# Optimization experiments

Measured on AMD Instinct MI355X. Metric: run time of the kernel, lower is better.

Reference implementation:

```python
import jax, jax.numpy as jnp
import numpy as np

ORDER = 3  # polynomial filter order


def _sketch_conv(x, A, W, b, coeffs):
    # z = A @ (x W + b); out = sum_d coeffs[d-1] * z**d  (Horner-free power accumulation)
    z = A @ (x @ W + b)            # [N, out_c]
    p = z
    acc = coeffs[0] * z
    for d in range(1, ORDER):      # small fixed loop over polynomial order
        p = p * z
        acc = acc + coeffs[d] * p
    return acc


def setup_inputs() -> dict:
    key = jax.random.key(0)
    ks = jax.random.split(key, 12)
    N, C_IN, C_H, C_OUT = 8192, 128, 64, 40
    nf_mats = jax.random.normal(ks[0], (N, C_IN), dtype=jnp.float32)
    # scale by 1/sqrt(N) so polynomial powers stay O(1)
    conv_mats = jax.random.normal(ks[1], (N, N), dtype=jnp.float32) / np.float32(np.sqrt(N))
    def lin(k, fi, fo):
        kw, kb = jax.random.split(k)
        W = jax.random.normal(kw, (fi, fo), dtype=jnp.float32) / np.float32(np.sqrt(fi))
        b = jax.random.normal(kb, (fo,), dtype=jnp.float32) * np.float32(0.01)
        return W, b
    W1, b1 = lin(ks[2], C_IN, C_H)
    W2, b2 = lin(ks[3], C_H, C_H)
    W3, b3 = lin(ks[4], C_H, C_OUT)
    base = jnp.array([1.0, 0.0, 0.0], dtype=jnp.float32)
    c1 = base + jax.random.normal(ks[5], (ORDER,), dtype=jnp.float32) * 0.05
    c2 = base + jax.random.normal(ks[6], (ORDER,), dtype=jnp.float32) * 0.05
    c3 = base + jax.random.normal(ks[7], (ORDER,), dtype=jnp.float32) * 0.05
    return {"nf_mats": nf_mats, "conv_mats": conv_mats,
            "W1": W1, "b1": b1, "c1": c1,
            "W2": W2, "b2": b2, "c2": c2,
            "W3": W3, "b3": b3, "c3": c3}


def reference(nf_mats, conv_mats, W1, b1, c1, W2, b2, c2, W3, b3, c3):
    # SketchGCN eval-mode forward: batchnorm=False, dropout inactive.
    x = _sketch_conv(nf_mats, conv_mats, W1, b1, c1)      # first layer
    x = x + _sketch_conv(x, conv_mats, W2, b2, c2)        # residual middle layer
    return _sketch_conv(x, conv_mats, W3, b3, c3)         # output layer
```

## Files before the change

kernel.cpp:

```cpp
#include <hip/hip_runtime.h>
#include <stdint.h>

typedef __bf16 bf16x8 __attribute__((ext_vector_type(8)));
typedef float f32x4 __attribute__((ext_vector_type(4)));

using gvoid = const __attribute__((address_space(1))) void;
using lvoid = __attribute__((address_space(3))) void;

__device__ __forceinline__ unsigned short f2bf(float f) {
    union { float f; unsigned u; } x; x.f = f;
    unsigned u = x.u;
    u += 0x7FFFu + ((u >> 16) & 1u);
    return (unsigned short)(u >> 16);
}
__device__ __forceinline__ unsigned pack2(float lo, float hi) {
    return ((unsigned)f2bf(hi) << 16) | (unsigned)f2bf(lo);
}

template <int CIN>
__global__ __launch_bounds__(256) void small_gemm(const float* __restrict__ X,
                                                  const float* __restrict__ W,
                                                  const float* __restrict__ b,
                                                  int cout,
                                                  unsigned short* __restrict__ Yt) {
    __shared__ float Xs[64 * (CIN + 1)];
    __shared__ float Ws[CIN * 64];
    __shared__ float bs[64];
    const int t = threadIdx.x;
    const int i0 = blockIdx.x * 64;

    for (int e = t; e < 64 * CIN; e += 256) {
        int r = e / CIN, c = e % CIN;
        Xs[r * (CIN + 1) + c] = X[(size_t)(i0 + r) * CIN + c];
    }
    for (int e = t; e < CIN * 64; e += 256) {
        int k = e >> 6, j = e & 63;
        Ws[e] = (j < cout) ? W[k * cout + j] : 0.0f;
    }
    if (t < 64) bs[t] = (t < cout) ? b[t] : 0.0f;
    __syncthreads();

    const int i = t & 63;
    const int jg = t >> 6;
    float acc[16];
#pragma unroll
    for (int jj = 0; jj < 16; ++jj) acc[jj] = 0.0f;

    for (int k = 0; k < CIN; ++k) {
        float xv = Xs[i * (CIN + 1) + k];
        const float4* wr = (const float4*)&Ws[k * 64 + jg * 16];
#pragma unroll
        for (int q = 0; q < 4; ++q) {
            float4 w = wr[q];
            acc[q * 4 + 0] += xv * w.x;
            acc[q * 4 + 1] += xv * w.y;
            acc[q * 4 + 2] += xv * w.z;
            acc[q * 4 + 3] += xv * w.w;
        }
    }
#pragma unroll
    for (int jj = 0; jj < 16; ++jj) {
        int j = jg * 16 + jj;
        Yt[(size_t)j * 8192 + i0 + i] = f2bf(acc[jj] + bs[j]);
    }
}

template <int CONV>
__global__ __launch_bounds__(256) void big_gemm(const float* __restrict__ Afp,
                                                unsigned short* __restrict__ Ab,
                                                const unsigned short* __restrict__ Yt,
                                                float* __restrict__ P) {
    __shared__ unsigned short As[2][128 * 64];
    __shared__ unsigned short Bs[2][64 * 64];
    const int t = threadIdx.x;
    const int lane = t & 63, wid = t >> 6;
    const int lane15 = lane & 15, lane4 = lane >> 4;
    const int wm = wid >> 1, wn = wid & 1;
    const int row0 = blockIdx.x * 128;
    const int kbase = blockIdx.y * 1024;

    f32x4 acc[4][2];
    const f32x4 z4 = {0.f, 0.f, 0.f, 0.f};
#pragma unroll
    for (int m = 0; m < 4; ++m)
#pragma unroll
        for (int n = 0; n < 2; ++n) acc[m][n] = z4;

    float4 ra[4][2];

    auto loadA_regs = [&](int kt) {
#pragma unroll
        for (int ii = 0; ii < 4; ++ii) {
            int p = ii * 256 + t;
            int r = p >> 3, cl = p & 7;
            const float* gp = Afp + (size_t)(row0 + r) * 8192 + kt + cl * 8;
            ra[ii][0] = *(const float4*)gp;
            ra[ii][1] = *(const float4*)(gp + 4);
        }
    };
    auto writeA = [&](int nb, int kt) {
#pragma unroll
        for (int ii = 0; ii < 4; ++ii) {
            int p = ii * 256 + t;
            int r = p >> 3, cl = p & 7;
            uint4 ch;
            ch.x = pack2(ra[ii][0].x, ra[ii][0].y);
            ch.y = pack2(ra[ii][0].z, ra[ii][0].w);
            ch.z = pack2(ra[ii][1].x, ra[ii][1].y);
            ch.w = pack2(ra[ii][1].z, ra[ii][1].w);
            *(uint4*)&As[nb][((r << 3) | (cl ^ (r & 7))) << 3] = ch;
            *(uint4*)&Ab[(size_t)(row0 + r) * 8192 + kt + cl * 8] = ch;
        }
    };
    auto stageA = [&](int nb, int kt) {
#pragma unroll
        for (int ii = 0; ii < 4; ++ii) {
            int p = ii * 256 + wid * 64 + lane;
            int r = p >> 3;
            int c = (p & 7) ^ (r & 7);
            const unsigned short* gp = Ab + (size_t)(row0 + r) * 8192 + (kt + c * 8);
            unsigned short* lp = &As[nb][(ii * 256 + wid * 64) * 8];
            __builtin_amdgcn_global_load_lds((gvoid*)gp, (lvoid*)lp, 16, 0, 0);
        }
    };
    auto stageB = [&](int nb, int kt) {
#pragma unroll
        for (int ii = 0; ii < 2; ++ii) {
            int q = ii * 256 + wid * 64 + lane;
            int n = q >> 3;
            int c = (q & 7) ^ (n & 7);
            const unsigned short* gp = Yt + (size_t)n * 8192 + (kt + c * 8);
            unsigned short* lp = &Bs[nb][(ii * 256 + wid * 64) * 8];
            __builtin_amdgcn_global_load_lds((gvoid*)gp, (lvoid*)lp, 16, 0, 0);
        }
    };

    if (CONV) {
        loadA_regs(kbase);
        stageB(0, kbase);
        writeA(0, kbase);
    } else {
        stageA(0, kbase);
        stageB(0, kbase);
    }
    __syncthreads();

    int buf = 0;
    const int NIT = 16;
    for (int tt = 0; tt < NIT; ++tt) {
        const bool pre = (tt + 1 < NIT);
        const int kt1 = kbase + (tt + 1) * 64;
        if (pre) {
            if (CONV) {
                loadA_regs(kt1);
                stageB(buf ^ 1, kt1);
            } else {
                stageA(buf ^ 1, kt1);
                stageB(buf ^ 1, kt1);
            }
        }
#pragma unroll
        for (int ks = 0; ks < 2; ++ks) {
            bf16x8 af[4], bfr[2];
#pragma unroll
            for (int m = 0; m < 4; ++m) {
                int r = wm * 64 + m * 16 + lane15;
                int c = ks * 4 + lane4;
                af[m] = *(const bf16x8*)&As[buf][((r << 3) | (c ^ (r & 7))) << 3];
            }
#pragma unroll
            for (int n = 0; n < 2; ++n) {
                int rn = wn * 32 + n * 16 + lane15;
                int c = ks * 4 + lane4;
                bfr[n] = *(const bf16x8*)&Bs[buf][((rn << 3) | (c ^ (rn & 7))) << 3];
            }
#pragma unroll
            for (int m = 0; m < 4; ++m)
#pragma unroll
                for (int n = 0; n < 2; ++n)
                    acc[m][n] = __builtin_amdgcn_mfma_f32_16x16x32_bf16(
                        af[m], bfr[n], acc[m][n], 0, 0, 0);
        }
        if (CONV && pre) writeA(buf ^ 1, kt1);
        __syncthreads();
        buf ^= 1;
    }

    float* Po = P + (size_t)blockIdx.y * (8192 * 64);
#pragma unroll
    for (int m = 0; m < 4; ++m) {
        int r = row0 + wm * 64 + m * 16 + lane4 * 4;
#pragma unroll
        for (int n = 0; n < 2; ++n) {
            int cc = wn * 32 + n * 16 + lane15;
#pragma unroll
            for (int q = 0; q < 4; ++q)
                Po[(size_t)(r + q) * 64 + cc] = acc[m][n][q];
        }
    }
}

template <int MODE>
__global__ __launch_bounds__(256) void fused_reduce(const float* __restrict__ P,
                                                    const float* __restrict__ cf,
                                                    const float* __restrict__ Wn,
                                                    const float* __restrict__ bn,
                                                    int cout,
                                                    float* __restrict__ X1,
                                                    unsigned short* __restrict__ Yt) {
    __shared__ float Xs[64 * 65];
    __shared__ float Ws[64 * 64];
    __shared__ float bs[64];
    const int t = threadIdx.x;
    const int i0 = blockIdx.x * 64;
    const size_t NT = 8192 * 64;

    for (int e = t; e < 64 * 64; e += 256) {
        int k = e >> 6, j = e & 63;
        Ws[e] = (j < cout) ? Wn[k * cout + j] : 0.0f;
    }
    if (t < 64) bs[t] = (t < cout) ? bn[t] : 0.0f;
    const float c0 = cf[0], c1 = cf[1], c2 = cf[2];

    for (int s = 0; s < 16; ++s) {
        int e = s * 256 + t;
        int i = e >> 6, j = e & 63;
        size_t base = (size_t)(i0 + i) * 64 + j;
        float z = 0.f;
#pragma unroll
        for (int ks = 0; ks < 8; ++ks) z += P[ks * NT + base];
        float v = z * (c0 + z * (c1 + z * c2));
        if (MODE == 0) X1[base] = v;
        else           v += X1[base];
        Xs[i * 65 + j] = v;
    }
    __syncthreads();

    const int i = t & 63;
    const int jg = t >> 6;
    float acc[16];
#pragma unroll
    for (int jj = 0; jj < 16; ++jj) acc[jj] = 0.0f;
    for (int k = 0; k < 64; ++k) {
        float xv = Xs[i * 65 + k];
        const float4* wr = (const float4*)&Ws[k * 64 + jg * 16];
#pragma unroll
        for (int q = 0; q < 4; ++q) {
            float4 w = wr[q];
            acc[q * 4 + 0] += xv * w.x;
            acc[q * 4 + 1] += xv * w.y;
            acc[q * 4 + 2] += xv * w.z;
            acc[q * 4 + 3] += xv * w.w;
        }
    }
#pragma unroll
    for (int jj = 0; jj < 16; ++jj) {
        int j = jg * 16 + jj;
        Yt[(size_t)j * 8192 + i0 + i] = f2bf(acc[jj] + bs[j]);
    }
}

__global__ void reduce_out(const float* __restrict__ P, const float* __restrict__ cf,
                           float* __restrict__ out) {
    int t = blockIdx.x * 256 + threadIdx.x;
    const size_t NT = 8192 * 64;
    float z = 0.f;
#pragma unroll
    for (int ks = 0; ks < 8; ++ks) z += P[ks * NT + t];
    float c0 = cf[0], c1 = cf[1], c2 = cf[2];
    float v = z * (c0 + z * (c1 + z * c2));
    int i = t >> 6, j = t & 63;
    if (j < 40) out[(size_t)i * 40 + j] = v;
}

extern "C" void kernel_launch(void* const* d_in, const int* in_sizes, int n_in,
                              void* d_out, int out_size, void* d_ws, size_t ws_size,
                              hipStream_t stream) {
    const float* nf   = (const float*)d_in[0];
    const float* Amat = (const float*)d_in[1];
    const float* W1   = (const float*)d_in[2];
    const float* b1   = (const float*)d_in[3];
    const float* c1   = (const float*)d_in[4];
    const float* W2   = (const float*)d_in[5];
    const float* b2   = (const float*)d_in[6];
    const float* c2   = (const float*)d_in[7];
    const float* W3   = (const float*)d_in[8];
    const float* b3   = (const float*)d_in[9];
    const float* c3   = (const float*)d_in[10];
    float* out = (float*)d_out;

    char* ws = (char*)d_ws;
    unsigned short* Abf = (unsigned short*)(ws);
    unsigned short* Yt  = (unsigned short*)(ws + 134217728);
    float* X1           = (float*)(ws + 135266304);
    float* Pp           = (float*)(ws + 137363456);

    small_gemm<128><<<128, 256, 0, stream>>>(nf, W1, b1, 64, Yt);
    big_gemm<1><<<dim3(64, 8), 256, 0, stream>>>(Amat, Abf, Yt, Pp);
    fused_reduce<0><<<128, 256, 0, stream>>>(Pp, c1, W2, b2, 64, X1, Yt);

    big_gemm<0><<<dim3(64, 8), 256, 0, stream>>>(nullptr, Abf, Yt, Pp);
    fused_reduce<1><<<128, 256, 0, stream>>>(Pp, c2, W3, b3, 40, X1, Yt);

    big_gemm<0><<<dim3(64, 8), 256, 0, stream>>>(nullptr, Abf, Yt, Pp);
    reduce_out<<<2048, 256, 0, stream>>>(Pp, c3, out);
}
```

Before: 212.9 us.

## Halve GEMM row tiles for more blocks and vectorize reduction kernels

The row tile of big_gemm drops from 128 to 64, which doubles the grid to 1024 blocks, and launch bounds are added to raise occupancy across the 256 CUs. small_gemm and fused_reduce also use 32-row tiles to double their block counts. The split-K partial-sum reductions in fused_reduce and reduce_out now use float4 loads and stores. Smaller GEMM tiles reload each B tile twice as often, since B reuse per A-load halves, which adds L2 traffic for the bf16 adjacency matrix stream.

```diff
diff --git a/kernel.cpp b/kernel.cpp
--- a/kernel.cpp
+++ b/kernel.cpp
@@ -23,13 +23,13 @@
                                                   const float* __restrict__ b,
                                                   int cout,
                                                   unsigned short* __restrict__ Yt) {
-    __shared__ float Xs[64 * (CIN + 1)];
+    __shared__ float Xs[32 * (CIN + 1)];
     __shared__ float Ws[CIN * 64];
     __shared__ float bs[64];
     const int t = threadIdx.x;
-    const int i0 = blockIdx.x * 64;
-
-    for (int e = t; e < 64 * CIN; e += 256) {
+    const int i0 = blockIdx.x * 32;
+
+    for (int e = t; e < 32 * CIN; e += 256) {
         int r = e / CIN, c = e % CIN;
         Xs[r * (CIN + 1) + c] = X[(size_t)(i0 + r) * CIN + c];
     }
@@ -40,57 +40,55 @@
     if (t < 64) bs[t] = (t < cout) ? b[t] : 0.0f;
     __syncthreads();
 
-    const int i = t & 63;
-    const int jg = t >> 6;
-    float acc[16];
-#pragma unroll
-    for (int jj = 0; jj < 16; ++jj) acc[jj] = 0.0f;
+    const int i = t & 31;
+    const int jg = t >> 5;
+    float acc[8];
+#pragma unroll
+    for (int jj = 0; jj < 8; ++jj) acc[jj] = 0.0f;
 
     for (int k = 0; k < CIN; ++k) {
         float xv = Xs[i * (CIN + 1) + k];
-        const float4* wr = (const float4*)&Ws[k * 64 + jg * 16];
-#pragma unroll
-        for (int q = 0; q < 4; ++q) {
-            float4 w = wr[q];
-            acc[q * 4 + 0] += xv * w.x;
-            acc[q * 4 + 1] += xv * w.y;
-            acc[q * 4 + 2] += xv * w.z;
-            acc[q * 4 + 3] += xv * w.w;
-        }
-    }
-#pragma unroll
-    for (int jj = 0; jj < 16; ++jj) {
-        int j = jg * 16 + jj;
+        const float4* wr = (const float4*)&Ws[k * 64 + jg * 8];
+        float4 w0 = wr[0], w1 = wr[1];
+        acc[0] += xv * w0.x; acc[1] += xv * w0.y;
+        acc[2] += xv * w0.z; acc[3] += xv * w0.w;
+        acc[4] += xv * w1.x; acc[5] += xv * w1.y;
+        acc[6] += xv * w1.z; acc[7] += xv * w1.w;
+    }
+#pragma unroll
+    for (int jj = 0; jj < 8; ++jj) {
+        int j = jg * 8 + jj;
         Yt[(size_t)j * 8192 + i0 + i] = f2bf(acc[jj] + bs[j]);
     }
 }
 
 template <int CONV>
-__global__ __launch_bounds__(256) void big_gemm(const float* __restrict__ Afp,
-                                                unsigned short* __restrict__ Ab,
-                                                const unsigned short* __restrict__ Yt,
-                                                float* __restrict__ P) {
-    __shared__ unsigned short As[2][128 * 64];
+__global__ __launch_bounds__(256, CONV ? 3 : 4)
+void big_gemm(const float* __restrict__ Afp,
+              unsigned short* __restrict__ Ab,
+              const unsigned short* __restrict__ Yt,
+              float* __restrict__ P) {
+    __shared__ unsigned short As[2][64 * 64];
     __shared__ unsigned short Bs[2][64 * 64];
     const int t = threadIdx.x;
     const int lane = t & 63, wid = t >> 6;
     const int lane15 = lane & 15, lane4 = lane >> 4;
     const int wm = wid >> 1, wn = wid & 1;
-    const int row0 = blockIdx.x * 128;
+    const int row0 = blockIdx.x * 64;
     const int kbase = blockIdx.y * 1024;
 
-    f32x4 acc[4][2];
+    f32x4 acc[2][2];
     const f32x4 z4 = {0.f, 0.f, 0.f, 0.f};
 #pragma unroll
-    for (int m = 0; m < 4; ++m)
+    for (int m = 0; m < 2; ++m)
 #pragma unroll
         for (int n = 0; n < 2; ++n) acc[m][n] = z4;
 
-    float4 ra[4][2];
+    float4 ra[2][2];
 
     auto loadA_regs = [&](int kt) {
 #pragma unroll
-        for (int ii = 0; ii < 4; ++ii) {
+        for (int ii = 0; ii < 2; ++ii) {
             int p = ii * 256 + t;
             int r = p >> 3, cl = p & 7;
             const float* gp = Afp + (size_t)(row0 + r) * 8192 + kt + cl * 8;
@@ -100,7 +98,7 @@
     };
     auto writeA = [&](int nb, int kt) {
 #pragma unroll
-        for (int ii = 0; ii < 4; ++ii) {
+        for (int ii = 0; ii < 2; ++ii) {
             int p = ii * 256 + t;
             int r = p >> 3, cl = p & 7;
             uint4 ch;
@@ -114,7 +112,7 @@
     };
     auto stageA = [&](int nb, int kt) {
 #pragma unroll
-        for (int ii = 0; ii < 4; ++ii) {
+        for (int ii = 0; ii < 2; ++ii) {
             int p = ii * 256 + wid * 64 + lane;
             int r = p >> 3;
             int c = (p & 7) ^ (r & 7);
@@ -161,10 +159,10 @@
         }
 #pragma unroll
         for (int ks = 0; ks < 2; ++ks) {
-            bf16x8 af[4], bfr[2];
-#pragma unroll
-            for (int m = 0; m < 4; ++m) {
-                int r = wm * 64 + m * 16 + lane15;
+            bf16x8 af[2], bfr[2];
+#pragma unroll
+            for (int m = 0; m < 2; ++m) {
+                int r = wm * 32 + m * 16 + lane15;
                 int c = ks * 4 + lane4;
                 af[m] = *(const bf16x8*)&As[buf][((r << 3) | (c ^ (r & 7))) << 3];
             }
@@ -175,7 +173,7 @@
                 bfr[n] = *(const bf16x8*)&Bs[buf][((rn << 3) | (c ^ (rn & 7))) << 3];
             }
 #pragma unroll
-            for (int m = 0; m < 4; ++m)
+            for (int m = 0; m < 2; ++m)
 #pragma unroll
                 for (int n = 0; n < 2; ++n)
                     acc[m][n] = __builtin_amdgcn_mfma_f32_16x16x32_bf16(
@@ -188,8 +186,8 @@
 
     float* Po = P + (size_t)blockIdx.y * (8192 * 64);
 #pragma unroll
-    for (int m = 0; m < 4; ++m) {
-        int r = row0 + wm * 64 + m * 16 + lane4 * 4;
+    for (int m = 0; m < 2; ++m) {
+        int r = row0 + wm * 32 + m * 16 + lane4 * 4;
 #pragma unroll
         for (int n = 0; n < 2; ++n) {
             int cc = wn * 32 + n * 16 + lane15;
@@ -208,12 +206,14 @@
                                                     int cout,
                                                     float* __restrict__ X1,
                                                     unsigned short* __restrict__ Yt) {
-    __shared__ float Xs[64 * 65];
+    __shared__ float Xs[64 * 33];
     __shared__ float Ws[64 * 64];
     __shared__ float bs[64];
     const int t = threadIdx.x;
-    const int i0 = blockIdx.x * 64;
-    const size_t NT = 8192 * 64;
+    const int i0 = blockIdx.x * 32;
+    const int NT4 = 8192 * 64 / 4;
+    const float4* P4 = (const float4*)P;
+    float4* X14 = (float4*)X1;
 
     for (int e = t; e < 64 * 64; e += 256) {
         int k = e >> 6, j = e & 63;
@@ -222,55 +222,75 @@
     if (t < 64) bs[t] = (t < cout) ? bn[t] : 0.0f;
     const float c0 = cf[0], c1 = cf[1], c2 = cf[2];
 
-    for (int s = 0; s < 16; ++s) {
-        int e = s * 256 + t;
-        int i = e >> 6, j = e & 63;
-        size_t base = (size_t)(i0 + i) * 64 + j;
-        float z = 0.f;
-#pragma unroll
-        for (int ks = 0; ks < 8; ++ks) z += P[ks * NT + base];
-        float v = z * (c0 + z * (c1 + z * c2));
-        if (MODE == 0) X1[base] = v;
-        else           v += X1[base];
-        Xs[i * 65 + j] = v;
+#pragma unroll
+    for (int s = 0; s < 2; ++s) {
+        int e4 = s * 256 + t;
+        int i = e4 >> 4, jc = e4 & 15;
+        int base4 = (i0 + i) * 16 + jc;
+        float4 z = {0.f, 0.f, 0.f, 0.f};
+#pragma unroll
+        for (int ks = 0; ks < 8; ++ks) {
+            float4 p = P4[(size_t)ks * NT4 + base4];
+            z.x += p.x; z.y += p.y; z.z += p.z; z.w += p.w;
+        }
+        float4 v;
+        v.x = z.x * (c0 + z.x * (c1 + z.x * c2));
+        v.y = z.y * (c0 + z.y * (c1 + z.y * c2));
+        v.z = z.z * (c0 + z.z * (c1 + z.z * c2));
+        v.w = z.w * (c0 + z.w * (c1 + z.w * c2));
+        if (MODE == 0) {
+            X14[base4] = v;
+        } else {
+            float4 xr = X14[base4];
+            v.x += xr.x; v.y += xr.y; v.z += xr.z; v.w += xr.w;
+        }
+        Xs[(jc * 4 + 0) * 33 + i] = v.x;
+        Xs[(jc * 4 + 1) * 33 + i] = v.y;
+        Xs[(jc * 4 + 2) * 33 + i] = v.z;
+        Xs[(jc * 4 + 3) * 33 + i] = v.w;
     }
     __syncthreads();
 
-    const int i = t & 63;
-    const int jg = t >> 6;
-    float acc[16];
-#pragma unroll
-    for (int jj = 0; jj < 16; ++jj) acc[jj] = 0.0f;
+    const int i = t & 31;
+    const int jg = t >> 5;
+    float acc[8];
+#pragma unroll
+    for (int jj = 0; jj < 8; ++jj) acc[jj] = 0.0f;
     for (int k = 0; k < 64; ++k) {
-        float xv = Xs[i * 65 + k];
-        const float4* wr = (const float4*)&Ws[k * 64 + jg * 16];
-#pragma unroll
-        for (int q = 0; q < 4; ++q) {
-            float4 w = wr[q];
-            acc[q * 4 + 0] += xv * w.x;
-            acc[q * 4 + 1] += xv * w.y;
-            acc[q * 4 + 2] += xv * w.z;
-            acc[q * 4 + 3] += xv * w.w;
-        }
-    }
-#pragma unroll
-    for (int jj = 0; jj < 16; ++jj) {
-        int j = jg * 16 + jj;
+        float xv = Xs[k * 33 + i];
+        const float4* wr = (const float4*)&Ws[k * 64 + jg * 8];
+        float4 w0 = wr[0], w1 = wr[1];
+        acc[0] += xv * w0.x; acc[1] += xv * w0.y;
+        acc[2] += xv * w0.z; acc[3] += xv * w0.w;
+        acc[4] += xv * w1.x; acc[5] += xv * w1.y;
+        acc[6] += xv * w1.z; acc[7] += xv * w1.w;
+    }
+#pragma unroll
+    for (int jj = 0; jj < 8; ++jj) {
+        int j = jg * 8 + jj;
         Yt[(size_t)j * 8192 + i0 + i] = f2bf(acc[jj] + bs[j]);
     }
 }
 
 __global__ void reduce_out(const float* __restrict__ P, const float* __restrict__ cf,
                            float* __restrict__ out) {
-    int t = blockIdx.x * 256 + threadIdx.x;
-    const size_t NT = 8192 * 64;
-    float z = 0.f;
-#pragma unroll
-    for (int ks = 0; ks < 8; ++ks) z += P[ks * NT + t];
+    int e4 = blockIdx.x * 256 + threadIdx.x;
+    const int NT4 = 8192 * 64 / 4;
+    const float4* P4 = (const float4*)P;
+    float4 z = {0.f, 0.f, 0.f, 0.f};
+#pragma unroll
+    for (int ks = 0; ks < 8; ++ks) {
+        float4 p = P4[(size_t)ks * NT4 + e4];
+        z.x += p.x; z.y += p.y; z.z += p.z; z.w += p.w;
+    }
     float c0 = cf[0], c1 = cf[1], c2 = cf[2];
-    float v = z * (c0 + z * (c1 + z * c2));
-    int i = t >> 6, j = t & 63;
-    if (j < 40) out[(size_t)i * 40 + j] = v;
+    float4 v;
+    v.x = z.x * (c0 + z.x * (c1 + z.x * c2));
+    v.y = z.y * (c0 + z.y * (c1 + z.y * c2));
+    v.z = z.z * (c0 + z.z * (c1 + z.z * c2));
+    v.w = z.w * (c0 + z.w * (c1 + z.w * c2));
+    int i = e4 >> 4, jc = e4 & 15;
+    if (jc < 10) ((float4*)out)[i * 10 + jc] = v;
 }
 
 extern "C" void kernel_launch(void* const* d_in, const int* in_sizes, int n_in,
@@ -295,13 +315,13 @@
     float* X1           = (float*)(ws + 135266304);
     float* Pp           = (float*)(ws + 137363456);
 
-    small_gemm<128><<<128, 256, 0, stream>>>(nf, W1, b1, 64, Yt);
-    big_gemm<1><<<dim3(64, 8), 256, 0, stream>>>(Amat, Abf, Yt, Pp);
-    fused_reduce<0><<<128, 256, 0, stream>>>(Pp, c1, W2, b2, 64, X1, Yt);
-
-    big_gemm<0><<<dim3(64, 8), 256, 0, stream>>>(nullptr, Abf, Yt, Pp);
-    fused_reduce<1><<<128, 256, 0, stream>>>(Pp, c2, W3, b3, 40, X1, Yt);
-
-    big_gemm<0><<<dim3(64, 8), 256, 0, stream>>>(nullptr, Abf, Yt, Pp);
-    reduce_out<<<2048, 256, 0, stream>>>(Pp, c3, out);
-}
+    small_gemm<128><<<256, 256, 0, stream>>>(nf, W1, b1, 64, Yt);
+    big_gemm<1><<<dim3(128, 8), 256, 0, stream>>>(Amat, Abf, Yt, Pp);
+    fused_reduce<0><<<256, 256, 0, stream>>>(Pp, c1, W2, b2, 64, X1, Yt);
+
+    big_gemm<0><<<dim3(128, 8), 256, 0, stream>>>(nullptr, Abf, Yt, Pp);
+    fused_reduce<1><<<256, 256, 0, stream>>>(Pp, c2, W3, b3, 40, X1, Yt);
+
+    big_gemm<0><<<dim3(128, 8), 256, 0, stream>>>(nullptr, Abf, Yt, Pp);
+    reduce_out<<<512, 256, 0, stream>>>(Pp, c3, out);
+}
```

Result: slower. 223.4 us (+5.0%).
